# Kernel tuning notes

Measured on AMD Instinct MI355X. Metric: run time of the kernel, lower is better.

The kernel has to match this reference:

```python
import jax, jax.numpy as jnp
import numpy as np

B = 65536          # batch
NUM_RULES = 4      # num_rules (init default)
NUM_VARS = 2       # effective num_variables after op-slot handling
RULE_DIM = 64
VAR_DIM = 100      # per-variable feature dim
HIDDEN_DIM = 2 * VAR_DIM  # 200, pinned by primary[:, :100] cat -> rule_mlp(hidden_dim)
D_K = 32           # variable_rule_select key dim
MLP_HID = 128      # GroupMLP hidden width


def _uniform(key, shape, fan_in):
    bound = 1.0 / np.sqrt(fan_in)
    return jax.random.uniform(key, shape, minval=-bound, maxval=bound, dtype=jnp.float32)


def setup_inputs() -> dict:
    key = jax.random.key(0)
    ks = jax.random.split(key, 7)
    return {
        "hidden": jax.random.normal(ks[0], (B, 3, VAR_DIM), dtype=jnp.float32),
        # rule embeddings: nn.Parameter(torch.randn(1, num_rules, rule_dim))
        "rule_emb": jax.random.normal(ks[1], (1, NUM_RULES, RULE_DIM), dtype=jnp.float32),
        # SelectAttention shared query (share_query=True -> nn.Linear(rule_dim, d_k))
        "Wq": _uniform(ks[2], (RULE_DIM, D_K), RULE_DIM),
        "bq": _uniform(ks[3], (D_K,), RULE_DIM),
        # SelectAttention per-variable key proj (GroupLinearLayer(hidden_dim, d_k, num_vars))
        "Wk": _uniform(ks[4], (NUM_VARS, HIDDEN_DIM, D_K), HIDDEN_DIM),
        # rule_mlp = GroupMLP(hidden_dim, hidden_dim//2, num_rules): two grouped linears
        "W1": _uniform(ks[5], (NUM_RULES, HIDDEN_DIM, MLP_HID), HIDDEN_DIM),
        "W2": _uniform(ks[6], (NUM_RULES, MLP_HID, VAR_DIM), MLP_HID),
    }


def argmax_onehot(x):
    # ArgMax.forward: scatter 1 at argmax along dim 1 (eval-mode hard selection)
    return jax.nn.one_hot(jnp.argmax(x, axis=1), x.shape[1], dtype=x.dtype)


def reference(hidden, rule_emb, Wq, bq, Wk, W1, W2):
    b = hidden.shape[0]
    # build operand representations: op slot broadcast onto both operands
    op = jnp.repeat(hidden[:, 2:3, :], NUM_VARS, axis=1)            # (B, 2, 100)
    h = jnp.concatenate([hidden[:, :NUM_VARS, :], op], axis=-1)    # (B, 2, 200)

    rule_e = jnp.broadcast_to(rule_emb, (b, NUM_RULES, RULE_DIM))   # (B, 4, 64)

    # SelectAttention(rule_emb, hidden): shared query linear, grouped key linear
    read = rule_e @ Wq + bq                                         # (B, 4, 32)
    write = jnp.einsum('bvd,vdk->bvk', h, Wk)                       # (B, 2, 32)
    scores = jnp.einsum('brk,bvk->brv', read, write) / jnp.sqrt(jnp.float32(D_K))  # (B,4,2)

    # eval path: hard ArgMax one-hot over flattened (rule, variable) pairs
    mask = argmax_onehot(scores.reshape(b, -1)).reshape(b, NUM_RULES, NUM_VARS)
    mask = jnp.transpose(mask, (0, 2, 1))                           # (B, vars, rules)

    variable_mask = jnp.sum(mask, axis=2, keepdims=True)            # (B, 2, 1)
    rule_mask = jnp.sum(mask, axis=1)[:, :, None]                   # (B, 4, 1)

    primary = jnp.sum(h * variable_mask, axis=1)                    # (B, 200)
    context = jnp.sum(h * (1.0 - variable_mask), axis=1)            # (B, 200)

    rule_mlp_input = jnp.concatenate(
        [primary[:, :VAR_DIM], context[:, :VAR_DIM]], axis=1)       # (B, 200)

    # grouped rule MLP applied per rule, then gated by rule_mask
    x = jnp.broadcast_to(rule_mlp_input[:, None, :], (b, NUM_RULES, HIDDEN_DIM))
    x = jax.nn.relu(jnp.einsum('bnd,ndk->bnk', x, W1))              # (B, 4, 128)
    x = jnp.einsum('bnd,ndk->bnk', x, W2)                           # (B, 4, 100)
    out = jnp.sum(x * rule_mask, axis=1)                            # (B, 100)
    return out
```

## Files before the change

### kernel.cpp

```cpp
#include <hip/hip_runtime.h>
#include <hip/hip_bf16.h>

#define B_TOTAL 65536
#define NR 4
#define VD 100
#define HD 200
#define DK 32
#define MH 128
#define RD 64

typedef __attribute__((ext_vector_type(8))) short bf16x8;
typedef __attribute__((ext_vector_type(4))) float f32x4;

static __device__ inline unsigned short f2bf(float x) {
    __hip_bfloat16 h = __float2bfloat16(x);
    return __builtin_bit_cast(unsigned short, h);
}

#define WS_GC    0
#define WS_CNT   19200
#define WS_LIST  19456
#define WS_VB    543744
#define WS_W1F   609280
#define WS_W2F   838656

__global__ __launch_bounds__(256) void k0_prep(
    const float* __restrict__ rule_emb, const float* __restrict__ Wq,
    const float* __restrict__ bq, const float* __restrict__ Wk,
    double* __restrict__ Gc, int* __restrict__ cnt)
{
    int tid = threadIdx.x;
    if (tid < NR) cnt[tid] = 0;

    __shared__ double readS[NR * DK];
    if (tid < NR * DK) {
        int r = tid >> 5, k = tid & 31;
        double a = (double)bq[k];
        for (int d = 0; d < RD; ++d)
            a += (double)rule_emb[r * RD + d] * (double)Wq[d * DK + k];
        readS[tid] = a;
    }
    __syncthreads();

    for (int idx = tid; idx < 100 * 16; idx += 256) {
        int dd = idx >> 4, c = idx & 15;
        int isB = (c >> 3) & 1, v = (c >> 2) & 1, r = c & 3;
        int row = v * HD + isB * 100 + dd;
        double g = 0.0;
        for (int k = 0; k < DK; ++k)
            g += (double)Wk[row * DK + k] * readS[r * DK + k];
        Gc[idx] = g;
    }
}

__global__ __launch_bounds__(256) void k0_wfrag(
    const float* __restrict__ W1, const float* __restrict__ W2,
    unsigned short* __restrict__ W1f, unsigned short* __restrict__ W2f)
{
    int i = blockIdx.x * 256 + threadIdx.x;
    if (i < 114688) {
        int r = i / 28672, rem = i % 28672;
        int ks = rem / 4096, rem2 = rem % 4096;
        int n = rem2 >> 9, l = (rem2 >> 3) & 63, j = rem2 & 7;
        int k = ks * 32 + ((l >> 4) << 3) + j;
        int c = n * 16 + (l & 15);
        float v = (k < HD) ? W1[((size_t)r * HD + k) * MH + c] : 0.f;
        W1f[i] = f2bf(v);
    } else if (i < 114688 + 57344) {
        int t = i - 114688;
        int r = t / 14336, rem = t % 14336;
        int ks = rem / 3584, rem2 = rem % 3584;
        int n = rem2 >> 9, l = (rem2 >> 3) & 63, j = rem2 & 7;
        int k = ks * 32 + ((l >> 4) << 3) + j;
        int c = n * 16 + (l & 15);
        float v = (c < VD) ? W2[((size_t)r * MH + k) * VD + c] : 0.f;
        W2f[t] = f2bf(v);
    }
}

__global__ __launch_bounds__(256) void k1_select(
    const float* __restrict__ hidden, const double* __restrict__ Gc,
    int* __restrict__ cnt, unsigned short* __restrict__ list16,
    unsigned char* __restrict__ vbyte)
{
    __shared__ double Gs[100 * 16];
    __shared__ int lcnt[NR];
    __shared__ int lbase[NR];
    int tid = threadIdx.x;
    for (int i = tid; i < 1600; i += 256) Gs[i] = Gc[i];
    if (tid < NR) lcnt[tid] = 0;
    __syncthreads();

    int b = blockIdx.x * 256 + tid;
    const float4* h0 = (const float4*)(hidden + (size_t)b * 300);
    const float4* h1 = h0 + 25;
    const float4* h2 = h0 + 50;

    double acc[16];
#pragma unroll
    for (int c = 0; c < 16; ++c) acc[c] = 0.0;

    for (int t0 = 0; t0 < 25; t0 += 5) {
        float4 va[5], vb[5], vc[5];
#pragma unroll
        for (int u = 0; u < 5; ++u) { va[u] = h0[t0 + u]; vb[u] = h1[t0 + u]; vc[u] = h2[t0 + u]; }
#pragma unroll
        for (int u = 0; u < 5; ++u) {
            float e0[4] = {va[u].x, va[u].y, va[u].z, va[u].w};
            float e1[4] = {vb[u].x, vb[u].y, vb[u].z, vb[u].w};
            float e2[4] = {vc[u].x, vc[u].y, vc[u].z, vc[u].w};
#pragma unroll
            for (int q = 0; q < 4; ++q) {
                int dd = (t0 + u) * 4 + q;
                const double* g = &Gs[dd * 16];
                double x0 = (double)e0[q], x1 = (double)e1[q], x2 = (double)e2[q];
#pragma unroll
                for (int r = 0; r < 4; ++r) acc[r]     = fma(x0, g[r],     acc[r]);
#pragma unroll
                for (int r = 0; r < 4; ++r) acc[4 + r] = fma(x1, g[4 + r], acc[4 + r]);
#pragma unroll
                for (int r = 0; r < 8; ++r) acc[8 + r] = fma(x2, g[8 + r], acc[8 + r]);
            }
        }
    }

    double sc[8];
#pragma unroll
    for (int r = 0; r < 4; ++r) {
        sc[r * 2]     = acc[r]     + acc[8 + r];
        sc[r * 2 + 1] = acc[4 + r] + acc[12 + r];
    }
    int best = 0; double bv = sc[0];
#pragma unroll
    for (int p = 1; p < 8; ++p) if (sc[p] > bv) { bv = sc[p]; best = p; }
    int r = best >> 1, v = best & 1;

    vbyte[b] = (unsigned char)v;
    int pos = atomicAdd(&lcnt[r], 1);
    __syncthreads();
    if (tid < NR) lbase[tid] = atomicAdd(&cnt[tid], lcnt[tid]);
    __syncthreads();
    list16[r * B_TOTAL + lbase[r] + pos] = (unsigned short)b;
}

__global__ __launch_bounds__(256) void k2_mlp(
    const float* __restrict__ hidden,
    const unsigned short* __restrict__ W1f, const unsigned short* __restrict__ W2f,
    const int* __restrict__ cnt, const unsigned short* __restrict__ list16,
    const unsigned char* __restrict__ vbyte, float* __restrict__ out)
{
    int r = blockIdx.y;
    int nb = cnt[r];
    int m0 = blockIdx.x * 64;
    if (m0 >= nb) return;
    int me = nb - m0; if (me > 64) me = 64;

    __shared__ __align__(16) unsigned short shbuf[64 * 232];
    __shared__ int ent[64];

    int tid = threadIdx.x;
    int wave = tid >> 6, lane = tid & 63;
    int lr = lane & 15, lk = lane >> 4;
    int wrow0 = wave * 16;

    if (tid < 64) {
        int idx = m0 + tid; if (idx > nb - 1) idx = nb - 1;
        int b = list16[r * B_TOTAL + idx];
        int v = vbyte[b];
        ent[tid] = (b << 1) | v;
    }
    __syncthreads();

    {
        int e = tid >> 2, hh = (tid >> 1) & 1, t = tid & 1;
        int en = ent[e];
        int b = en >> 1, v = en & 1;
        int seg = hh ? (1 - v) : v;
        int q0 = t * 12;
        const float4* src = (const float4*)(hidden + (size_t)b * 300 + seg * 100) + q0;
        float4 hv[13];
#pragma unroll
        for (int u = 0; u < 13; ++u) hv[u] = src[u];
#pragma unroll
        for (int u = 0; u < 13; ++u) {
            ushort4 o;
            o.x = f2bf(hv[u].x); o.y = f2bf(hv[u].y);
            o.z = f2bf(hv[u].z); o.w = f2bf(hv[u].w);
            *(ushort4*)&shbuf[e * 232 + (hh * 25 + q0 + u) * 4] = o;
        }
    }
    {
        int row = tid >> 2, part = tid & 3;
        bf16x8 z = {0, 0, 0, 0, 0, 0, 0, 0};
        *(bf16x8*)&shbuf[row * 232 + 200 + part * 8] = z;
    }
    __syncthreads();

    const unsigned short* W1f_r = W1f + (size_t)r * 28672;
    f32x4 acc1[8];
#pragma unroll
    for (int n = 0; n < 8; ++n) acc1[n] = (f32x4){0.f, 0.f, 0.f, 0.f};

#pragma unroll
    for (int ks = 0; ks < 7; ++ks) {
        bf16x8 a0 = *(const bf16x8*)&shbuf[(wrow0 + lr) * 232 + ks * 32 + lk * 8];
#pragma unroll
        for (int n = 0; n < 8; ++n) {
            bf16x8 bfr = *(const bf16x8*)&W1f_r[(size_t)(ks * 8 + n) * 512 + lane * 8];
            acc1[n] = __builtin_amdgcn_mfma_f32_16x16x32_bf16(a0, bfr, acc1[n], 0, 0, 0);
        }
    }

    __syncthreads();

#pragma unroll
    for (int n = 0; n < 8; ++n)
#pragma unroll
        for (int j = 0; j < 4; ++j) {
            float v = fmaxf(acc1[n][j], 0.f);
            int row = wrow0 + lk * 4 + j;
            shbuf[row * 136 + n * 16 + lr] = f2bf(v);
        }
    __syncthreads();

    const unsigned short* W2f_r = W2f + (size_t)r * 14336;
    f32x4 acc2[7];
#pragma unroll
    for (int n = 0; n < 7; ++n) acc2[n] = (f32x4){0.f, 0.f, 0.f, 0.f};

#pragma unroll
    for (int ks = 0; ks < 4; ++ks) {
        bf16x8 a0 = *(const bf16x8*)&shbuf[(wrow0 + lr) * 136 + ks * 32 + lk * 8];
#pragma unroll
        for (int n = 0; n < 7; ++n) {
            bf16x8 bfr = *(const bf16x8*)&W2f_r[(size_t)(ks * 7 + n) * 512 + lane * 8];
            acc2[n] = __builtin_amdgcn_mfma_f32_16x16x32_bf16(a0, bfr, acc2[n], 0, 0, 0);
        }
    }

#pragma unroll
    for (int n = 0; n < 7; ++n) {
        int col = n * 16 + lr;
        if (col < VD) {
#pragma unroll
            for (int j = 0; j < 4; ++j) {
                int e = wrow0 + lk * 4 + j;
                if (e < me) {
                    int b = ent[e] >> 1;
                    out[(size_t)b * VD + col] = acc2[n][j];
                }
            }
        }
    }
}

extern "C" void kernel_launch(void* const* d_in, const int* in_sizes, int n_in,
                              void* d_out, int out_size, void* d_ws, size_t ws_size,
                              hipStream_t stream) {
    (void)in_sizes; (void)n_in; (void)out_size; (void)ws_size;
    const float* hidden   = (const float*)d_in[0];
    const float* rule_emb = (const float*)d_in[1];
    const float* Wq       = (const float*)d_in[2];
    const float* bq       = (const float*)d_in[3];
    const float* Wk       = (const float*)d_in[4];
    const float* W1       = (const float*)d_in[5];
    const float* W2       = (const float*)d_in[6];
    float* out = (float*)d_out;

    char* ws = (char*)d_ws;
    double* Gc             = (double*)(ws + WS_GC);
    int* cnt               = (int*)(ws + WS_CNT);
    unsigned short* list16 = (unsigned short*)(ws + WS_LIST);
    unsigned char* vbyte   = (unsigned char*)(ws + WS_VB);
    unsigned short* W1f    = (unsigned short*)(ws + WS_W1F);
    unsigned short* W2f    = (unsigned short*)(ws + WS_W2F);

    k0_prep<<<1, 256, 0, stream>>>(rule_emb, Wq, bq, Wk, Gc, cnt);
    k0_wfrag<<<672, 256, 0, stream>>>(W1, W2, W1f, W2f);
    k1_select<<<256, 256, 0, stream>>>(hidden, Gc, cnt, list16, vbyte);
    k2_mlp<<<dim3(1024, NR), 256, 0, stream>>>(hidden, W1f, W2f, cnt, list16, vbyte, out);
}
```

Measured before the change: 84.70 us.

## Stage hidden rows in shared memory and split select dot products across four lanes

```diff
diff --git a/kernel.cpp b/kernel.cpp
--- a/kernel.cpp
+++ b/kernel.cpp
@@ -11,6 +11,7 @@
 
 typedef __attribute__((ext_vector_type(8))) short bf16x8;
 typedef __attribute__((ext_vector_type(4))) float f32x4;
+typedef __attribute__((ext_vector_type(2))) double f64x2;
 
 static __device__ inline unsigned short f2bf(float x) {
     __hip_bfloat16 h = __float2bfloat16(x);
@@ -83,64 +84,105 @@
     int* __restrict__ cnt, unsigned short* __restrict__ list16,
     unsigned char* __restrict__ vbyte)
 {
-    __shared__ double Gs[100 * 16];
+    __shared__ float hs[64 * 300];
+    __shared__ double Gsp[4 * 402];
+    __shared__ double pacc[64][4][18];
     __shared__ int lcnt[NR];
     __shared__ int lbase[NR];
+
     int tid = threadIdx.x;
-    for (int i = tid; i < 1600; i += 256) Gs[i] = Gc[i];
+    for (int i = tid; i < 1600; i += 256) {
+        int dd = i >> 4, c = i & 15;
+        int qk = dd / 25, u = dd - qk * 25;
+        Gsp[qk * 402 + u * 16 + c] = Gc[i];
+    }
     if (tid < NR) lcnt[tid] = 0;
     __syncthreads();
 
-    int b = blockIdx.x * 256 + tid;
-    const float4* h0 = (const float4*)(hidden + (size_t)b * 300);
-    const float4* h1 = h0 + 25;
-    const float4* h2 = h0 + 50;
-
-    double acc[16];
-#pragma unroll
-    for (int c = 0; c < 16; ++c) acc[c] = 0.0;
-
-    for (int t0 = 0; t0 < 25; t0 += 5) {
-        float4 va[5], vb[5], vc[5];
-#pragma unroll
-        for (int u = 0; u < 5; ++u) { va[u] = h0[t0 + u]; vb[u] = h1[t0 + u]; vc[u] = h2[t0 + u]; }
-#pragma unroll
-        for (int u = 0; u < 5; ++u) {
-            float e0[4] = {va[u].x, va[u].y, va[u].z, va[u].w};
-            float e1[4] = {vb[u].x, vb[u].y, vb[u].z, vb[u].w};
-            float e2[4] = {vc[u].x, vc[u].y, vc[u].z, vc[u].w};
-#pragma unroll
-            for (int q = 0; q < 4; ++q) {
-                int dd = (t0 + u) * 4 + q;
-                const double* g = &Gs[dd * 16];
-                double x0 = (double)e0[q], x1 = (double)e1[q], x2 = (double)e2[q];
-#pragma unroll
-                for (int r = 0; r < 4; ++r) acc[r]     = fma(x0, g[r],     acc[r]);
-#pragma unroll
-                for (int r = 0; r < 4; ++r) acc[4 + r] = fma(x1, g[4 + r], acc[4 + r]);
-#pragma unroll
-                for (int r = 0; r < 8; ++r) acc[8 + r] = fma(x2, g[8 + r], acc[8 + r]);
+    int e = tid >> 2, qk = tid & 3;
+    const f64x2* Gq = (const f64x2*)&Gsp[qk * 402];
+
+    for (int t = 0; t < 4; ++t) {
+        int rowbase = blockIdx.x * 256 + t * 64;
+
+        const float4* src4 = (const float4*)(hidden + (size_t)rowbase * 300);
+        float4* hs4 = (float4*)hs;
+#pragma unroll
+        for (int k = 0; k < 19; ++k) {
+            int idx = tid + k * 256;
+            if (idx < 4800) hs4[idx] = src4[idx];
+        }
+        __syncthreads();
+
+        double acc[16];
+#pragma unroll
+        for (int c = 0; c < 16; ++c) acc[c] = 0.0;
+
+        const float* hrow = &hs[e * 300 + qk * 25];
+#pragma unroll
+        for (int u = 0; u < 25; ++u) {
+            double x0 = (double)hrow[u];
+            double x1 = (double)hrow[100 + u];
+            double x2 = (double)hrow[200 + u];
+            const f64x2* g = Gq + u * 8;
+            f64x2 g0 = g[0], g1 = g[1];
+            acc[0] = fma(x0, g0[0], acc[0]);
+            acc[1] = fma(x0, g0[1], acc[1]);
+            acc[2] = fma(x0, g1[0], acc[2]);
+            acc[3] = fma(x0, g1[1], acc[3]);
+            f64x2 g2 = g[2], g3 = g[3];
+            acc[4] = fma(x1, g2[0], acc[4]);
+            acc[5] = fma(x1, g2[1], acc[5]);
+            acc[6] = fma(x1, g3[0], acc[6]);
+            acc[7] = fma(x1, g3[1], acc[7]);
+            f64x2 g4 = g[4], g5 = g[5], g6 = g[6], g7 = g[7];
+            acc[8]  = fma(x2, g4[0], acc[8]);
+            acc[9]  = fma(x2, g4[1], acc[9]);
+            acc[10] = fma(x2, g5[0], acc[10]);
+            acc[11] = fma(x2, g5[1], acc[11]);
+            acc[12] = fma(x2, g6[0], acc[12]);
+            acc[13] = fma(x2, g6[1], acc[13]);
+            acc[14] = fma(x2, g7[0], acc[14]);
+            acc[15] = fma(x2, g7[1], acc[15]);
+        }
+        if (qk != 0) {
+#pragma unroll
+            for (int c = 0; c < 16; ++c) pacc[e][qk][c] = acc[c];
+        }
+        __syncthreads();
+
+        int r = 0, v = 0, pos = 0;
+        if (qk == 0) {
+#pragma unroll
+            for (int q = 1; q < 4; ++q)
+#pragma unroll
+                for (int c = 0; c < 16; ++c) acc[c] += pacc[e][q][c];
+
+            double sc[8];
+#pragma unroll
+            for (int rr = 0; rr < 4; ++rr) {
+                sc[rr * 2]     = acc[rr]     + acc[8 + rr];
+                sc[rr * 2 + 1] = acc[4 + rr] + acc[12 + rr];
             }
-        }
-    }
-
-    double sc[8];
-#pragma unroll
-    for (int r = 0; r < 4; ++r) {
-        sc[r * 2]     = acc[r]     + acc[8 + r];
-        sc[r * 2 + 1] = acc[4 + r] + acc[12 + r];
-    }
-    int best = 0; double bv = sc[0];
-#pragma unroll
-    for (int p = 1; p < 8; ++p) if (sc[p] > bv) { bv = sc[p]; best = p; }
-    int r = best >> 1, v = best & 1;
-
-    vbyte[b] = (unsigned char)v;
-    int pos = atomicAdd(&lcnt[r], 1);
-    __syncthreads();
-    if (tid < NR) lbase[tid] = atomicAdd(&cnt[tid], lcnt[tid]);
-    __syncthreads();
-    list16[r * B_TOTAL + lbase[r] + pos] = (unsigned short)b;
+            int best = 0; double bv = sc[0];
+#pragma unroll
+            for (int p = 1; p < 8; ++p) if (sc[p] > bv) { bv = sc[p]; best = p; }
+            r = best >> 1; v = best & 1;
+
+            vbyte[rowbase + e] = (unsigned char)v;
+            pos = atomicAdd(&lcnt[r], 1);
+        }
+        __syncthreads();
+
+        if (tid < NR) {
+            lbase[tid] = atomicAdd(&cnt[tid], lcnt[tid]);
+            lcnt[tid] = 0;
+        }
+        __syncthreads();
+
+        if (qk == 0) list16[r * B_TOTAL + lbase[r] + pos] = (unsigned short)(rowbase + e);
+        __syncthreads();
+    }
 }
 
 __global__ __launch_bounds__(256) void k2_mlp(
```

New measurement: 74.70 us. 1.13x faster.

## Split select scoring across four threads per row with 4x more blocks

Applied to the files above, without the earlier changes.

```diff
diff --git a/kernel.cpp b/kernel.cpp
--- a/kernel.cpp
+++ b/kernel.cpp
@@ -11,6 +11,7 @@
 
 typedef __attribute__((ext_vector_type(8))) short bf16x8;
 typedef __attribute__((ext_vector_type(4))) float f32x4;
+typedef __attribute__((ext_vector_type(2))) double f64x2;
 
 static __device__ inline unsigned short f2bf(float x) {
     __hip_bfloat16 h = __float2bfloat16(x);
@@ -83,64 +84,86 @@
     int* __restrict__ cnt, unsigned short* __restrict__ list16,
     unsigned char* __restrict__ vbyte)
 {
-    __shared__ double Gs[100 * 16];
+    __shared__ double pacc[64][17];
     __shared__ int lcnt[NR];
     __shared__ int lbase[NR];
     int tid = threadIdx.x;
-    for (int i = tid; i < 1600; i += 256) Gs[i] = Gc[i];
     if (tid < NR) lcnt[tid] = 0;
     __syncthreads();
 
-    int b = blockIdx.x * 256 + tid;
-    const float4* h0 = (const float4*)(hidden + (size_t)b * 300);
-    const float4* h1 = h0 + 25;
-    const float4* h2 = h0 + 50;
-
-    double acc[16];
-#pragma unroll
-    for (int c = 0; c < 16; ++c) acc[c] = 0.0;
-
-    for (int t0 = 0; t0 < 25; t0 += 5) {
-        float4 va[5], vb[5], vc[5];
-#pragma unroll
-        for (int u = 0; u < 5; ++u) { va[u] = h0[t0 + u]; vb[u] = h1[t0 + u]; vc[u] = h2[t0 + u]; }
-#pragma unroll
-        for (int u = 0; u < 5; ++u) {
-            float e0[4] = {va[u].x, va[u].y, va[u].z, va[u].w};
-            float e1[4] = {vb[u].x, vb[u].y, vb[u].z, vb[u].w};
-            float e2[4] = {vc[u].x, vc[u].y, vc[u].z, vc[u].w};
-#pragma unroll
-            for (int q = 0; q < 4; ++q) {
-                int dd = (t0 + u) * 4 + q;
-                const double* g = &Gs[dd * 16];
-                double x0 = (double)e0[q], x1 = (double)e1[q], x2 = (double)e2[q];
-#pragma unroll
-                for (int r = 0; r < 4; ++r) acc[r]     = fma(x0, g[r],     acc[r]);
-#pragma unroll
-                for (int r = 0; r < 4; ++r) acc[4 + r] = fma(x1, g[4 + r], acc[4 + r]);
-#pragma unroll
-                for (int r = 0; r < 8; ++r) acc[8 + r] = fma(x2, g[8 + r], acc[8 + r]);
+    int e = tid >> 2, qk = tid & 3;
+    int row = blockIdx.x * 64 + e;
+    int seg = (qk < 2) ? qk : 2;
+    const float4* src = (const float4*)(hidden + (size_t)row * 300 + seg * 100);
+    const f64x2* G2 = (const f64x2*)Gc;
+
+    double acc[4];
+#pragma unroll
+    for (int c = 0; c < 4; ++c) acc[c] = 0.0;
+
+    {
+        float4 hv[13];
+#pragma unroll
+        for (int u = 0; u < 13; ++u) hv[u] = src[u];
+#pragma unroll
+        for (int u = 0; u < 13; ++u) {
+            float he[4] = {hv[u].x, hv[u].y, hv[u].z, hv[u].w};
+#pragma unroll
+            for (int j = 0; j < 4; ++j) {
+                int dd = u * 4 + j;
+                double x = (double)he[j];
+                f64x2 g0 = G2[dd * 8 + qk * 2], g1 = G2[dd * 8 + qk * 2 + 1];
+                acc[0] = fma(x, g0[0], acc[0]);
+                acc[1] = fma(x, g0[1], acc[1]);
+                acc[2] = fma(x, g1[0], acc[2]);
+                acc[3] = fma(x, g1[1], acc[3]);
             }
         }
     }
-
-    double sc[8];
-#pragma unroll
-    for (int r = 0; r < 4; ++r) {
-        sc[r * 2]     = acc[r]     + acc[8 + r];
-        sc[r * 2 + 1] = acc[4 + r] + acc[12 + r];
-    }
-    int best = 0; double bv = sc[0];
-#pragma unroll
-    for (int p = 1; p < 8; ++p) if (sc[p] > bv) { bv = sc[p]; best = p; }
-    int r = best >> 1, v = best & 1;
-
-    vbyte[b] = (unsigned char)v;
-    int pos = atomicAdd(&lcnt[r], 1);
+    {
+        float4 hv[12];
+#pragma unroll
+        for (int u = 0; u < 12; ++u) hv[u] = src[13 + u];
+#pragma unroll
+        for (int u = 0; u < 12; ++u) {
+            float he[4] = {hv[u].x, hv[u].y, hv[u].z, hv[u].w};
+#pragma unroll
+            for (int j = 0; j < 4; ++j) {
+                int dd = (13 + u) * 4 + j;
+                double x = (double)he[j];
+                f64x2 g0 = G2[dd * 8 + qk * 2], g1 = G2[dd * 8 + qk * 2 + 1];
+                acc[0] = fma(x, g0[0], acc[0]);
+                acc[1] = fma(x, g0[1], acc[1]);
+                acc[2] = fma(x, g1[0], acc[2]);
+                acc[3] = fma(x, g1[1], acc[3]);
+            }
+        }
+    }
+
+#pragma unroll
+    for (int c = 0; c < 4; ++c) pacc[e][qk * 4 + c] = acc[c];
+    __syncthreads();
+
+    int r = 0, v = 0, pos = 0;
+    if (qk == 0) {
+        double sc[8];
+#pragma unroll
+        for (int rr = 0; rr < 4; ++rr) {
+            sc[rr * 2]     = acc[rr]          + pacc[e][8 + rr];
+            sc[rr * 2 + 1] = pacc[e][4 + rr]  + pacc[e][12 + rr];
+        }
+        int best = 0; double bv = sc[0];
+#pragma unroll
+        for (int p = 1; p < 8; ++p) if (sc[p] > bv) { bv = sc[p]; best = p; }
+        r = best >> 1; v = best & 1;
+
+        vbyte[row] = (unsigned char)v;
+        pos = atomicAdd(&lcnt[r], 1);
+    }
     __syncthreads();
     if (tid < NR) lbase[tid] = atomicAdd(&cnt[tid], lcnt[tid]);
     __syncthreads();
-    list16[r * B_TOTAL + lbase[r] + pos] = (unsigned short)b;
+    if (qk == 0) list16[r * B_TOTAL + lbase[r] + pos] = (unsigned short)row;
 }
 
 __global__ __launch_bounds__(256) void k2_mlp(
@@ -277,6 +300,6 @@
 
     k0_prep<<<1, 256, 0, stream>>>(rule_emb, Wq, bq, Wk, Gc, cnt);
     k0_wfrag<<<672, 256, 0, stream>>>(W1, W2, W1f, W2f);
-    k1_select<<<256, 256, 0, stream>>>(hidden, Gc, cnt, list16, vbyte);
+    k1_select<<<1024, 256, 0, stream>>>(hidden, Gc, cnt, list16, vbyte);
     k2_mlp<<<dim3(1024, NR), 256, 0, stream>>>(hidden, W1f, W2f, cnt, list16, vbyte, out);
 }
```

Measured after the change: 82.54 us. -2.6%, faster.

## Split selection scoring across 4 lanes per row group with shuffle reduction

Applied to the files above, without the earlier changes.

```diff
diff --git a/kernel.cpp b/kernel.cpp
--- a/kernel.cpp
+++ b/kernel.cpp
@@ -11,6 +11,7 @@
 
 typedef __attribute__((ext_vector_type(8))) short bf16x8;
 typedef __attribute__((ext_vector_type(4))) float f32x4;
+typedef __attribute__((ext_vector_type(2))) double f64x2;
 
 static __device__ inline unsigned short f2bf(float x) {
     __hip_bfloat16 h = __float2bfloat16(x);
@@ -83,64 +84,85 @@
     int* __restrict__ cnt, unsigned short* __restrict__ list16,
     unsigned char* __restrict__ vbyte)
 {
-    __shared__ double Gs[100 * 16];
     __shared__ int lcnt[NR];
     __shared__ int lbase[NR];
     int tid = threadIdx.x;
-    for (int i = tid; i < 1600; i += 256) Gs[i] = Gc[i];
     if (tid < NR) lcnt[tid] = 0;
     __syncthreads();
 
-    int b = blockIdx.x * 256 + tid;
-    const float4* h0 = (const float4*)(hidden + (size_t)b * 300);
-    const float4* h1 = h0 + 25;
-    const float4* h2 = h0 + 50;
-
-    double acc[16];
-#pragma unroll
-    for (int c = 0; c < 16; ++c) acc[c] = 0.0;
-
-    for (int t0 = 0; t0 < 25; t0 += 5) {
-        float4 va[5], vb[5], vc[5];
-#pragma unroll
-        for (int u = 0; u < 5; ++u) { va[u] = h0[t0 + u]; vb[u] = h1[t0 + u]; vc[u] = h2[t0 + u]; }
-#pragma unroll
-        for (int u = 0; u < 5; ++u) {
-            float e0[4] = {va[u].x, va[u].y, va[u].z, va[u].w};
-            float e1[4] = {vb[u].x, vb[u].y, vb[u].z, vb[u].w};
-            float e2[4] = {vc[u].x, vc[u].y, vc[u].z, vc[u].w};
-#pragma unroll
-            for (int q = 0; q < 4; ++q) {
-                int dd = (t0 + u) * 4 + q;
-                const double* g = &Gs[dd * 16];
-                double x0 = (double)e0[q], x1 = (double)e1[q], x2 = (double)e2[q];
-#pragma unroll
-                for (int r = 0; r < 4; ++r) acc[r]     = fma(x0, g[r],     acc[r]);
-#pragma unroll
-                for (int r = 0; r < 4; ++r) acc[4 + r] = fma(x1, g[4 + r], acc[4 + r]);
-#pragma unroll
-                for (int r = 0; r < 8; ++r) acc[8 + r] = fma(x2, g[8 + r], acc[8 + r]);
+    int cq = tid & 3;
+    int rowbase = blockIdx.x * 256 + (tid >> 2) * 4;
+    int seg = (cq < 2) ? cq : 2;
+    const f64x2* G2 = (const f64x2*)Gc;
+
+    double acc[4][4];
+#pragma unroll
+    for (int rr = 0; rr < 4; ++rr)
+#pragma unroll
+        for (int c = 0; c < 4; ++c) acc[rr][c] = 0.0;
+
+    for (int d0 = 0; d0 < 100; d0 += 4) {
+        f64x2 gb[8];
+#pragma unroll
+        for (int k = 0; k < 4; ++k) {
+            gb[k * 2]     = G2[(d0 + k) * 8 + cq * 2];
+            gb[k * 2 + 1] = G2[(d0 + k) * 8 + cq * 2 + 1];
+        }
+        float4 hb[4];
+#pragma unroll
+        for (int rr = 0; rr < 4; ++rr)
+            hb[rr] = *(const float4*)(hidden + (size_t)(rowbase + rr) * 300 + seg * 100 + d0);
+#pragma unroll
+        for (int rr = 0; rr < 4; ++rr) {
+            float he[4] = {hb[rr].x, hb[rr].y, hb[rr].z, hb[rr].w};
+#pragma unroll
+            for (int k = 0; k < 4; ++k) {
+                double x = (double)he[k];
+                acc[rr][0] = fma(x, gb[k * 2][0],     acc[rr][0]);
+                acc[rr][1] = fma(x, gb[k * 2][1],     acc[rr][1]);
+                acc[rr][2] = fma(x, gb[k * 2 + 1][0], acc[rr][2]);
+                acc[rr][3] = fma(x, gb[k * 2 + 1][1], acc[rr][3]);
             }
         }
     }
 
-    double sc[8];
-#pragma unroll
-    for (int r = 0; r < 4; ++r) {
-        sc[r * 2]     = acc[r]     + acc[8 + r];
-        sc[r * 2 + 1] = acc[4 + r] + acc[12 + r];
-    }
-    int best = 0; double bv = sc[0];
-#pragma unroll
-    for (int p = 1; p < 8; ++p) if (sc[p] > bv) { bv = sc[p]; best = p; }
-    int r = best >> 1, v = best & 1;
-
-    vbyte[b] = (unsigned char)v;
-    int pos = atomicAdd(&lcnt[r], 1);
+    int rsel[4], vsel[4], pos[4];
+#pragma unroll
+    for (int rr = 0; rr < 4; ++rr) {
+        double s0[4], s8[4];
+#pragma unroll
+        for (int j = 0; j < 4; ++j) {
+            double other = __shfl_xor(acc[rr][j], 2);
+            s0[j] = acc[rr][j] + other;
+        }
+#pragma unroll
+        for (int j = 0; j < 4; ++j) s8[j] = __shfl_xor(s0[j], 1);
+
+        double sc8[8];
+#pragma unroll
+        for (int j = 0; j < 4; ++j) { sc8[j * 2] = s0[j]; sc8[j * 2 + 1] = s8[j]; }
+        int best = 0; double bv = sc8[0];
+#pragma unroll
+        for (int p = 1; p < 8; ++p) if (sc8[p] > bv) { bv = sc8[p]; best = p; }
+        rsel[rr] = best >> 1; vsel[rr] = best & 1;
+    }
+
+    if (cq == 0) {
+#pragma unroll
+        for (int rr = 0; rr < 4; ++rr) {
+            vbyte[rowbase + rr] = (unsigned char)vsel[rr];
+            pos[rr] = atomicAdd(&lcnt[rsel[rr]], 1);
+        }
+    }
     __syncthreads();
     if (tid < NR) lbase[tid] = atomicAdd(&cnt[tid], lcnt[tid]);
     __syncthreads();
-    list16[r * B_TOTAL + lbase[r] + pos] = (unsigned short)b;
+    if (cq == 0) {
+#pragma unroll
+        for (int rr = 0; rr < 4; ++rr)
+            list16[rsel[rr] * B_TOTAL + lbase[rsel[rr]] + pos[rr]] =
+                (unsigned short)(rowbase + rr);
+    }
 }
 
 __global__ __launch_bounds__(256) void k2_mlp(
```

After: 84.11 us. No clear change (-0.7%).
